# Kernel optimization log

Hardware: AMD Instinct MI355X
Metric: run time of the kernel (lower is better)

Reference implementation:

```python
import jax, jax.numpy as jnp
import numpy as np

B, H, W, D = 8, 64, 64, 256   # batch, grid rows, grid cols, q_size==c_size
N = 1024                      # number of query/alignment points
R_WIN, C_WIN = 1, 2           # hardcoded window half-sizes from the module


def setup_inputs() -> dict:
    key = jax.random.key(0)
    k1, k2, k3, k4 = jax.random.split(key, 4)
    q = jax.random.normal(k1, (B, H, W, D), jnp.float32)
    c_t = jax.random.normal(k2, (B, N, D), jnp.float32)
    # float positions inside the grid: row in [0,H-1), col in [0,W-1)
    p_t = jax.random.uniform(k3, (B, N, 2), jnp.float32) * jnp.array([H - 1, W - 1], jnp.float32)
    W_a = jax.random.normal(k4, (D, D), jnp.float32) / np.sqrt(D)  # nn.Linear(q_size->c_size) weight [c,q]
    return {"q": q, "c_t": c_t, "p_t": p_t, "W_a": W_a}


def reference(q, c_t, p_t, W_a):
    Bq, Hh, Ww, Dd = q.shape
    rows, cols = Hh + 1, Ww + 1
    # ConstantPad2d((1,0,1,0), nan) on channels-first layout == pad top row & left col with NaN
    q_pad = jnp.pad(q.transpose(0, 3, 1, 2), ((0, 0), (0, 0), (1, 0), (1, 0)),
                    constant_values=jnp.nan)                      # [B,D,rows,cols]
    p0 = p_t[..., 0].astype(jnp.int32)
    p1 = p_t[..., 1].astype(jnp.int32)
    r = jnp.clip(p0[..., None] + jnp.arange(-R_WIN, R_WIN + 1) + 1, 0, rows) % rows  # [B,N,2R+1]
    c = jnp.clip(p1[..., None] + jnp.arange(-C_WIN, C_WIN + 1) + 1, 0, cols) % cols  # [B,N,2C+1]
    # flattened window indices, i (row offset) major, j (col offset) minor
    idx = (r[..., :, None] * cols + c[..., None, :]).reshape(Bq, r.shape[1], -1)     # [B,N,K]
    K = idx.shape[-1]
    q_flat = q_pad.reshape(Bq, Dd, rows * cols).transpose(0, 2, 1)                   # [B,rows*cols,D]
    qg = jnp.take_along_axis(q_flat, idx.reshape(Bq, -1, 1), axis=1)
    qg = qg.reshape(Bq, idx.shape[1], K, Dd)                                          # [B,N,K,D]
    nan_loc = jnp.isnan(qg[..., 0])                                                   # [B,N,K]
    qg = jnp.where(nan_loc[..., None], 0.0, qg)
    # Gaussian decay around the (float) predicted position
    rexp = jnp.exp(-2.0 * ((jnp.clip(r.astype(q.dtype) - 1, 0, None) - p_t[..., 0:1]) / R_WIN) ** 2)
    cexp = jnp.exp(-2.0 * ((jnp.clip(c.astype(q.dtype) - 1, 0, None) - p_t[..., 1:2]) / C_WIN) ** 2)
    expw = (rexp[..., :, None] * cexp[..., None, :]).reshape(Bq, r.shape[1], K)       # [B,N,K]
    # score: (W_a qg) . c_t per (b,n)
    Wa = jnp.einsum('bnkd,cd->bnkc', qg, W_a)
    a_t = jnp.einsum('bnkc,bnc->bnk', Wa, c_t)
    a_t = jnp.where(nan_loc, -jnp.inf, a_t)
    W_attn = jax.nn.softmax(a_t, axis=2) * expw
    return jnp.einsum('bnk,bnkd->bnd', W_attn, qg)                                    # [B,N,D]
```

## Files before the change

kernel.cpp:

```cpp
#include <hip/hip_runtime.h>
#include <math.h>

#define BATCH   8
#define HGRID   64
#define WGRID   64
#define DDIM    256
#define NPTS    1024
#define ROWS    65
#define COLS    65
#define KWIN    15
#define BN      (BATCH*NPTS)

#define PIDS_PER_BLK 16
#define THREADS      512
#define PR_PITCH     260

typedef __attribute__((ext_vector_type(8))) short bf16x8;
typedef __attribute__((ext_vector_type(4))) float f32x4;

__global__ __launch_bounds__(THREADS, 4) void fused_local_attn(
        const float* __restrict__ q,
        const float* __restrict__ c_t,
        const float* __restrict__ p_t,
        const float* __restrict__ W,
        float* __restrict__ out) {

    __shared__ __align__(16) float Pr[PIDS_PER_BLK][PR_PITCH];

    const int t    = threadIdx.x;
    const int w    = t >> 6;
    const int lane = t & 63;
    const int l15  = lane & 15;
    const int g    = lane >> 4;
    const int pid0 = blockIdx.x * PIDS_PER_BLK;
    const int dq   = w * 32;

    f32x4 acc0 = (f32x4)0.f;
    f32x4 acc1 = (f32x4)0.f;

    const float* ap  = &c_t[(size_t)(pid0 + l15) * DDIM + g * 8];
    const float* wp0 = &W[(size_t)(g * 8) * DDIM + dq + l15];
    const float* wp1 = wp0 + 16;

    #pragma unroll 2
    for (int kt = 0; kt < 8; ++kt) {
        const float4 a01 = *reinterpret_cast<const float4*>(ap + kt * 32);
        const float4 a23 = *reinterpret_cast<const float4*>(ap + kt * 32 + 4);
        const float af[8] = {a01.x, a01.y, a01.z, a01.w, a23.x, a23.y, a23.z, a23.w};
        union { bf16x8 v; unsigned u[4]; } AH, AL;
        #pragma unroll
        for (int i = 0; i < 4; ++i) {
            const unsigned u0 = __float_as_uint(af[2 * i]);
            const unsigned u1 = __float_as_uint(af[2 * i + 1]);
            AH.u[i] = __builtin_amdgcn_perm(u1, u0, 0x07060302u);
            const float l0 = af[2 * i]     - __uint_as_float(u0 & 0xFFFF0000u);
            const float l1 = af[2 * i + 1] - __uint_as_float(u1 & 0xFFFF0000u);
            AL.u[i] = __builtin_amdgcn_perm(__float_as_uint(l1), __float_as_uint(l0),
                                            0x07060302u);
        }

        #pragma unroll
        for (int df = 0; df < 2; ++df) {
            const float* wp = (df == 0) ? wp0 : wp1;
            float bf[8];
            #pragma unroll
            for (int i = 0; i < 8; ++i)
                bf[i] = wp[(size_t)(kt * 32 + i) * DDIM];
            union { bf16x8 v; unsigned u[4]; } BH, BL;
            #pragma unroll
            for (int i = 0; i < 4; ++i) {
                const unsigned u0 = __float_as_uint(bf[2 * i]);
                const unsigned u1 = __float_as_uint(bf[2 * i + 1]);
                BH.u[i] = __builtin_amdgcn_perm(u1, u0, 0x07060302u);
                const float l0 = bf[2 * i]     - __uint_as_float(u0 & 0xFFFF0000u);
                const float l1 = bf[2 * i + 1] - __uint_as_float(u1 & 0xFFFF0000u);
                BL.u[i] = __builtin_amdgcn_perm(__float_as_uint(l1), __float_as_uint(l0),
                                                0x07060302u);
            }
            f32x4 a = (df == 0) ? acc0 : acc1;
            a = __builtin_amdgcn_mfma_f32_16x16x32_bf16(AH.v, BH.v, a, 0, 0, 0);
            a = __builtin_amdgcn_mfma_f32_16x16x32_bf16(AH.v, BL.v, a, 0, 0, 0);
            a = __builtin_amdgcn_mfma_f32_16x16x32_bf16(AL.v, BH.v, a, 0, 0, 0);
            if (df == 0) acc0 = a; else acc1 = a;
        }
    }

    #pragma unroll
    for (int r = 0; r < 4; ++r) {
        Pr[g * 4 + r][dq +  0 + l15] = acc0[r];
        Pr[g * 4 + r][dq + 16 + l15] = acc1[r];
    }
    __syncthreads();

    #pragma unroll 1
    for (int pp = 0; pp < 2; ++pp) {
        const int pl  = w * 2 + pp;
        const int pid = pid0 + pl;
        const int b   = pid >> 10;
        const float2 ppos = *reinterpret_cast<const float2*>(&p_t[pid * 2]);
        const float p0f = ppos.x;
        const float p1f = ppos.y;
        const int p0 = (int)p0f;
        const int p1 = (int)p1f;

        const float4 pr = *reinterpret_cast<const float4*>(&Pr[pl][lane * 4]);

        float re[3], ce[5];
        int rowidx[3], colidx[5];
        #pragma unroll
        for (int i = 0; i < 3; ++i) {
            int rr = p0 + i;
            rr = rr > ROWS ? ROWS : rr;
            rr = (rr == ROWS) ? 0 : rr;
            rowidx[i] = rr;
            const float rf = (float)(rr - 1 > 0 ? rr - 1 : 0);
            const float dr = rf - p0f;
            re[i] = __expf(-2.0f * dr * dr);
        }
        #pragma unroll
        for (int j = 0; j < 5; ++j) {
            int cc = p1 + j - 1;
            cc = cc < 0 ? 0 : (cc > COLS ? COLS : cc);
            cc = (cc == COLS) ? 0 : cc;
            colidx[j] = cc;
            const float cf = (float)(cc - 1 > 0 ? cc - 1 : 0);
            const float dc = (cf - p1f) * 0.5f;
            ce[j] = __expf(-2.0f * dc * dc);
        }

        float4 qg[KWIN];
        float score[KWIN];
        unsigned vmask = 0;

        #pragma unroll
        for (int i = 0; i < 3; ++i) {
            #pragma unroll
            for (int j = 0; j < 5; ++j) {
                const int k  = i * 5 + j;
                const int rr = rowidx[i];
                const int cc = colidx[j];
                const bool valid = (rr != 0) && (cc != 0);
                float s = 0.f;
                float4 v = make_float4(0.f, 0.f, 0.f, 0.f);
                if (valid) {
                    v = *reinterpret_cast<const float4*>(
                        &q[((size_t)((b * HGRID + rr - 1) * WGRID + cc - 1)) * DDIM
                           + lane * 4]);
                    s = fmaf(v.x, pr.x, fmaf(v.y, pr.y, fmaf(v.z, pr.z, v.w * pr.w)));
                    vmask |= (1u << k);
                }
                qg[k] = v;
                score[k] = s;
            }
        }

        #pragma unroll
        for (int k = 0; k < KWIN; ++k) {
            float s = score[k];
            #pragma unroll
            for (int off = 32; off; off >>= 1) s += __shfl_xor(s, off, 64);
            score[k] = ((vmask >> k) & 1u) ? s : -INFINITY;
        }

        float mx = score[0];
        #pragma unroll
        for (int k = 1; k < KWIN; ++k) mx = fmaxf(mx, score[k]);
        float sum = 0.f;
        #pragma unroll
        for (int k = 0; k < KWIN; ++k) {
            const float e = __expf(score[k] - mx);
            score[k] = e;
            sum += e;
        }
        const float inv = 1.0f / sum;

        float ox = 0.f, oy = 0.f, oz = 0.f, ow = 0.f;
        #pragma unroll
        for (int i = 0; i < 3; ++i) {
            #pragma unroll
            for (int j = 0; j < 5; ++j) {
                const int k = i * 5 + j;
                const float wk = score[k] * inv * re[i] * ce[j];
                ox = fmaf(wk, qg[k].x, ox);
                oy = fmaf(wk, qg[k].y, oy);
                oz = fmaf(wk, qg[k].z, oz);
                ow = fmaf(wk, qg[k].w, ow);
            }
        }
        *reinterpret_cast<float4*>(&out[(size_t)pid * DDIM + lane * 4]) =
            make_float4(ox, oy, oz, ow);
    }
}

extern "C" void kernel_launch(void* const* d_in, const int* in_sizes, int n_in,
                              void* d_out, int out_size, void* d_ws, size_t ws_size,
                              hipStream_t stream) {
    const float* q   = (const float*)d_in[0];
    const float* c_t = (const float*)d_in[1];
    const float* p_t = (const float*)d_in[2];
    const float* W_a = (const float*)d_in[3];
    float* out = (float*)d_out;

    fused_local_attn<<<BN / PIDS_PER_BLK, THREADS, 0, stream>>>(q, c_t, p_t, W_a, out);
}
```

Measured before the change: 36.44 us.

## Halve points per block and use online softmax to cut register pressure

```diff
diff --git a/kernel.cpp b/kernel.cpp
--- a/kernel.cpp
+++ b/kernel.cpp
@@ -11,14 +11,14 @@
 #define KWIN    15
 #define BN      (BATCH*NPTS)
 
-#define PIDS_PER_BLK 16
+#define PIDS_PER_BLK 8
 #define THREADS      512
 #define PR_PITCH     260
 
 typedef __attribute__((ext_vector_type(8))) short bf16x8;
 typedef __attribute__((ext_vector_type(4))) float f32x4;
 
-__global__ __launch_bounds__(THREADS, 4) void fused_local_attn(
+__global__ __launch_bounds__(THREADS, 8) void fused_local_attn(
         const float* __restrict__ q,
         const float* __restrict__ c_t,
         const float* __restrict__ p_t,
@@ -38,11 +38,10 @@
     f32x4 acc0 = (f32x4)0.f;
     f32x4 acc1 = (f32x4)0.f;
 
-    const float* ap  = &c_t[(size_t)(pid0 + l15) * DDIM + g * 8];
+    const float* ap  = &c_t[(size_t)(pid0 + (l15 & 7)) * DDIM + g * 8];
     const float* wp0 = &W[(size_t)(g * 8) * DDIM + dq + l15];
     const float* wp1 = wp0 + 16;
 
-    #pragma unroll 2
     for (int kt = 0; kt < 8; ++kt) {
         const float4 a01 = *reinterpret_cast<const float4*>(ap + kt * 32);
         const float4 a23 = *reinterpret_cast<const float4*>(ap + kt * 32 + 4);
@@ -85,111 +84,82 @@
         }
     }
 
-    #pragma unroll
-    for (int r = 0; r < 4; ++r) {
-        Pr[g * 4 + r][dq +  0 + l15] = acc0[r];
-        Pr[g * 4 + r][dq + 16 + l15] = acc1[r];
+    if (g < 2) {
+        #pragma unroll
+        for (int r = 0; r < 4; ++r) {
+            Pr[g * 4 + r][dq +  0 + l15] = acc0[r];
+            Pr[g * 4 + r][dq + 16 + l15] = acc1[r];
+        }
     }
     __syncthreads();
 
-    #pragma unroll 1
-    for (int pp = 0; pp < 2; ++pp) {
-        const int pl  = w * 2 + pp;
-        const int pid = pid0 + pl;
-        const int b   = pid >> 10;
-        const float2 ppos = *reinterpret_cast<const float2*>(&p_t[pid * 2]);
-        const float p0f = ppos.x;
-        const float p1f = ppos.y;
-        const int p0 = (int)p0f;
-        const int p1 = (int)p1f;
+    const int pid = pid0 + w;
+    const int b   = pid >> 10;
+    const float2 ppos = *reinterpret_cast<const float2*>(&p_t[pid * 2]);
+    const float p0f = ppos.x;
+    const float p1f = ppos.y;
+    const int p0 = (int)p0f;
+    const int p1 = (int)p1f;
 
-        const float4 pr = *reinterpret_cast<const float4*>(&Pr[pl][lane * 4]);
+    const float4 pr = *reinterpret_cast<const float4*>(&Pr[w][lane * 4]);
 
-        float re[3], ce[5];
-        int rowidx[3], colidx[5];
-        #pragma unroll
-        for (int i = 0; i < 3; ++i) {
-            int rr = p0 + i;
-            rr = rr > ROWS ? ROWS : rr;
-            rr = (rr == ROWS) ? 0 : rr;
-            rowidx[i] = rr;
-            const float rf = (float)(rr - 1 > 0 ? rr - 1 : 0);
-            const float dr = rf - p0f;
-            re[i] = __expf(-2.0f * dr * dr);
-        }
+    float re[3], ce[5];
+    int rowidx[3], colidx[5];
+    #pragma unroll
+    for (int i = 0; i < 3; ++i) {
+        int rr = p0 + i;
+        rr = rr > ROWS ? ROWS : rr;
+        rr = (rr == ROWS) ? 0 : rr;
+        rowidx[i] = rr;
+        const float rf = (float)(rr - 1 > 0 ? rr - 1 : 0);
+        const float dr = rf - p0f;
+        re[i] = __expf(-2.0f * dr * dr);
+    }
+    #pragma unroll
+    for (int j = 0; j < 5; ++j) {
+        int cc = p1 + j - 1;
+        cc = cc < 0 ? 0 : (cc > COLS ? COLS : cc);
+        cc = (cc == COLS) ? 0 : cc;
+        colidx[j] = cc;
+        const float cf = (float)(cc - 1 > 0 ? cc - 1 : 0);
+        const float dc = (cf - p1f) * 0.5f;
+        ce[j] = __expf(-2.0f * dc * dc);
+    }
+
+    float m = -INFINITY;
+    float s = 0.f;
+    float ox = 0.f, oy = 0.f, oz = 0.f, ow = 0.f;
+
+    #pragma unroll
+    for (int i = 0; i < 3; ++i) {
         #pragma unroll
         for (int j = 0; j < 5; ++j) {
-            int cc = p1 + j - 1;
-            cc = cc < 0 ? 0 : (cc > COLS ? COLS : cc);
-            cc = (cc == COLS) ? 0 : cc;
-            colidx[j] = cc;
-            const float cf = (float)(cc - 1 > 0 ? cc - 1 : 0);
-            const float dc = (cf - p1f) * 0.5f;
-            ce[j] = __expf(-2.0f * dc * dc);
-        }
-
-        float4 qg[KWIN];
-        float score[KWIN];
-        unsigned vmask = 0;
-
-        #pragma unroll
-        for (int i = 0; i < 3; ++i) {
-            #pragma unroll
-            for (int j = 0; j < 5; ++j) {
-                const int k  = i * 5 + j;
-                const int rr = rowidx[i];
-                const int cc = colidx[j];
-                const bool valid = (rr != 0) && (cc != 0);
-                float s = 0.f;
-                float4 v = make_float4(0.f, 0.f, 0.f, 0.f);
-                if (valid) {
-                    v = *reinterpret_cast<const float4*>(
-                        &q[((size_t)((b * HGRID + rr - 1) * WGRID + cc - 1)) * DDIM
-                           + lane * 4]);
-                    s = fmaf(v.x, pr.x, fmaf(v.y, pr.y, fmaf(v.z, pr.z, v.w * pr.w)));
-                    vmask |= (1u << k);
-                }
-                qg[k] = v;
-                score[k] = s;
+            const int rr = rowidx[i];
+            const int cc = colidx[j];
+            if ((rr != 0) && (cc != 0)) {
+                const float4 v = *reinterpret_cast<const float4*>(
+                    &q[((size_t)((b * HGRID + rr - 1) * WGRID + cc - 1)) * DDIM
+                       + lane * 4]);
+                float sc = fmaf(v.x, pr.x, fmaf(v.y, pr.y, fmaf(v.z, pr.z, v.w * pr.w)));
+                #pragma unroll
+                for (int off = 32; off; off >>= 1) sc += __shfl_xor(sc, off, 64);
+                const float mn   = fmaxf(m, sc);
+                const float corr = __expf(m - mn);
+                const float e    = __expf(sc - mn);
+                const float ew   = e * re[i] * ce[j];
+                m = mn;
+                s = fmaf(s, corr, e);
+                ox = fmaf(ox, corr, ew * v.x);
+                oy = fmaf(oy, corr, ew * v.y);
+                oz = fmaf(oz, corr, ew * v.z);
+                ow = fmaf(ow, corr, ew * v.w);
             }
         }
+    }
 
-        #pragma unroll
-        for (int k = 0; k < KWIN; ++k) {
-            float s = score[k];
-            #pragma unroll
-            for (int off = 32; off; off >>= 1) s += __shfl_xor(s, off, 64);
-            score[k] = ((vmask >> k) & 1u) ? s : -INFINITY;
-        }
-
-        float mx = score[0];
-        #pragma unroll
-        for (int k = 1; k < KWIN; ++k) mx = fmaxf(mx, score[k]);
-        float sum = 0.f;
-        #pragma unroll
-        for (int k = 0; k < KWIN; ++k) {
-            const float e = __expf(score[k] - mx);
-            score[k] = e;
-            sum += e;
-        }
-        const float inv = 1.0f / sum;
-
-        float ox = 0.f, oy = 0.f, oz = 0.f, ow = 0.f;
-        #pragma unroll
-        for (int i = 0; i < 3; ++i) {
-            #pragma unroll
-            for (int j = 0; j < 5; ++j) {
-                const int k = i * 5 + j;
-                const float wk = score[k] * inv * re[i] * ce[j];
-                ox = fmaf(wk, qg[k].x, ox);
-                oy = fmaf(wk, qg[k].y, oy);
-                oz = fmaf(wk, qg[k].z, oz);
-                ow = fmaf(wk, qg[k].w, ow);
-            }
-        }
-        *reinterpret_cast<float4*>(&out[(size_t)pid * DDIM + lane * 4]) =
-            make_float4(ox, oy, oz, ow);
-    }
+    const float inv = 1.0f / s;
+    *reinterpret_cast<float4*>(&out[(size_t)pid * DDIM + lane * 4]) =
+        make_float4(ox * inv, oy * inv, oz * inv, ow * inv);
 }
 
 extern "C" void kernel_launch(void* const* d_in, const int* in_sizes, int n_in,
```

New measurement: 41.71 us. +14.4%, slower.
